# Kernel tuning notes

Hardware: AMD Instinct MI355X
Metric: run time of the kernel (lower is better)

Reference implementation:

```python
import jax, jax.numpy as jnp
import numpy as np


def setup_inputs() -> dict:
    key = jax.random.key(0)
    k1, k2, k3, k4 = jax.random.split(key, 4)
    B, H, S, D = 8, 32, 8192, 128
    query = jax.random.normal(k1, (B, H, 1, D), dtype=jnp.float32)
    key_cache = jax.random.normal(k2, (B, H, S, D), dtype=jnp.float32)
    value_cache = jax.random.normal(k3, (B, H, S, D), dtype=jnp.float32)
    W_out = jax.random.normal(k4, (H * D, H * D), dtype=jnp.float32) * (1.0 / np.sqrt(H * D))
    b_out = jnp.zeros((H * D,), dtype=jnp.float32)
    return {"query": query, "key_cache": key_cache, "value_cache": value_cache,
            "W_out": W_out, "b_out": b_out}


def reference(query, key_cache, value_cache, W_out, b_out):
    B, H, _, D = query.shape
    # scores: [B, H, 1, S]
    scores = jnp.einsum("bhqd,bhsd->bhqs", query, key_cache) / jnp.sqrt(
        jnp.asarray(D, dtype=query.dtype))
    probs = jax.nn.softmax(scores, axis=-1)
    # attn values: [B, H, 1, D]
    attn = jnp.einsum("bhqs,bhsd->bhqd", probs, value_cache)
    # [B, 1, H*D]
    attn = attn.transpose(0, 2, 1, 3).reshape(B, 1, H * D)
    # out_proj: x @ W^T + b (torch Linear convention)
    out = attn @ W_out.T + b_out
    return out
```

## Files before the change

### kernel.cpp

```cpp
#include <hip/hip_runtime.h>
#include <math.h>

#define TPB    256
#define CHUNK  1024
#define DHEAD  128
#define NB     8

__global__ __launch_bounds__(TPB) void attn_partial(
    const float* __restrict__ q, const float* __restrict__ kc,
    const float* __restrict__ vc, float* __restrict__ part,
    int S, int nsplit)
{
    const int bh    = blockIdx.x;
    const int split = blockIdx.y;
    const int tid   = threadIdx.x;
    const int s0    = split * CHUNK;

    __shared__ float sc[CHUNK];
    __shared__ float qs[DHEAD];
    __shared__ float red[8];
    __shared__ float accs[8][DHEAD];

    if (tid < DHEAD) qs[tid] = q[(size_t)bh * DHEAD + tid];
    __syncthreads();

    const int lane32 = tid & 31;
    const int grp    = tid >> 5;
    const float4 q4  = ((const float4*)qs)[lane32];
    const float scale = 0.088388347648318447f;

    const float* Kbase = kc + ((size_t)bh * S + s0) * DHEAD;
    for (int it = 0; it < CHUNK / 8; ++it) {
        const int row = it * 8 + grp;
        const float4 k4 = ((const float4*)(Kbase + (size_t)row * DHEAD))[lane32];
        float p = q4.x * k4.x + q4.y * k4.y + q4.z * k4.z + q4.w * k4.w;
        #pragma unroll
        for (int off = 16; off > 0; off >>= 1) p += __shfl_xor(p, off);
        if (lane32 == 0) sc[row] = p * scale;
    }
    __syncthreads();

    float m = -INFINITY;
    for (int i = tid; i < CHUNK; i += TPB) m = fmaxf(m, sc[i]);
    #pragma unroll
    for (int off = 32; off > 0; off >>= 1) m = fmaxf(m, __shfl_xor(m, off));
    if ((tid & 63) == 0) red[tid >> 6] = m;
    __syncthreads();
    m = fmaxf(fmaxf(red[0], red[1]), fmaxf(red[2], red[3]));

    float lsum = 0.f;
    for (int i = tid; i < CHUNK; i += TPB) {
        const float e = expf(sc[i] - m);
        sc[i] = e;
        lsum += e;
    }
    #pragma unroll
    for (int off = 32; off > 0; off >>= 1) lsum += __shfl_xor(lsum, off);
    if ((tid & 63) == 0) red[4 + (tid >> 6)] = lsum;
    __syncthreads();
    lsum = red[4] + red[5] + red[6] + red[7];

    const float* Vbase = vc + ((size_t)bh * S + s0) * DHEAD;
    float4 acc = make_float4(0.f, 0.f, 0.f, 0.f);
    const int sBeg = grp * (CHUNK / 8);
    for (int s = sBeg; s < sBeg + CHUNK / 8; ++s) {
        const float  p  = sc[s];
        const float4 v4 = ((const float4*)(Vbase + (size_t)s * DHEAD))[lane32];
        acc.x += p * v4.x; acc.y += p * v4.y;
        acc.z += p * v4.z; acc.w += p * v4.w;
    }
    ((float4*)accs[grp])[lane32] = acc;
    __syncthreads();

    float* P = part + ((size_t)bh * nsplit + split) * (DHEAD + 2);
    if (tid < DHEAD) {
        float a = 0.f;
        #pragma unroll
        for (int g = 0; g < 8; ++g) a += accs[g][tid];
        P[tid] = a;
    }
    if (tid == 0) { P[DHEAD] = m; P[DHEAD + 1] = lsum; }
}

__global__ __launch_bounds__(DHEAD) void attn_combine(
    const float* __restrict__ part, float* __restrict__ attn,
    int nsplit, int H)
{
    const int bh  = blockIdx.x;
    const int tid = threadIdx.x;
    const float* P = part + (size_t)bh * nsplit * (DHEAD + 2);

    float m = -INFINITY;
    for (int s = 0; s < nsplit; ++s)
        m = fmaxf(m, P[s * (DHEAD + 2) + DHEAD]);

    float l = 0.f, a = 0.f;
    for (int s = 0; s < nsplit; ++s) {
        const float w = expf(P[s * (DHEAD + 2) + DHEAD] - m);
        l += P[s * (DHEAD + 2) + DHEAD + 1] * w;
        a += P[s * (DHEAD + 2) + tid] * w;
    }
    attn[(size_t)bh * DHEAD + tid] = a / l;
}

__global__ __launch_bounds__(TPB) void out_proj(
    const float* __restrict__ attn, const float* __restrict__ W,
    const float* __restrict__ bias, float* __restrict__ out, int HD)
{
    const int j   = blockIdx.x;
    const int tid = threadIdx.x;
    const float4* Wr = (const float4*)(W + (size_t)j * HD);
    const int nv = HD >> 2;

    float acc[NB];
    #pragma unroll
    for (int b = 0; b < NB; ++b) acc[b] = 0.f;

    for (int i = tid; i < nv; i += TPB) {
        const float4 w4 = Wr[i];
        #pragma unroll
        for (int b = 0; b < NB; ++b) {
            const float4 a4 = ((const float4*)attn)[(size_t)b * nv + i];
            acc[b] += w4.x * a4.x + w4.y * a4.y + w4.z * a4.z + w4.w * a4.w;
        }
    }

    #pragma unroll
    for (int b = 0; b < NB; ++b) {
        #pragma unroll
        for (int off = 32; off > 0; off >>= 1)
            acc[b] += __shfl_xor(acc[b], off);
    }

    __shared__ float red[4][NB];
    if ((tid & 63) == 0) {
        #pragma unroll
        for (int b = 0; b < NB; ++b) red[tid >> 6][b] = acc[b];
    }
    __syncthreads();
    if (tid < NB) {
        const float r = red[0][tid] + red[1][tid] + red[2][tid] + red[3][tid];
        out[(size_t)tid * HD + j] = r + bias[j];
    }
}

extern "C" void kernel_launch(void* const* d_in, const int* in_sizes, int n_in,
                              void* d_out, int out_size, void* d_ws, size_t ws_size,
                              hipStream_t stream)
{
    const float* q    = (const float*)d_in[0];
    const float* kc   = (const float*)d_in[1];
    const float* vc   = (const float*)d_in[2];
    const float* W    = (const float*)d_in[3];
    const float* bias = (const float*)d_in[4];
    float* out = (float*)d_out;

    const int HD = in_sizes[4];
    const int B  = in_sizes[0] / HD;
    const int H  = HD / DHEAD;
    const int S  = in_sizes[1] / in_sizes[0];
    const int BH = B * H;
    const int nsplit = S / CHUNK;

    float* part = (float*)d_ws;
    float* attn = part + (size_t)BH * nsplit * (DHEAD + 2);

    attn_partial<<<dim3(BH, nsplit), TPB, 0, stream>>>(q, kc, vc, part, S, nsplit);
    attn_combine<<<BH, DHEAD, 0, stream>>>(part, attn, nsplit, H);
    out_proj<<<HD, TPB, 0, stream>>>(attn, W, bias, out, HD);
}
```

Baseline: 401.9 us.

## Fuse split combine into partial kernel via atomic counter; widen out_proj rows

Removes the separate combine kernel: each partial block bumps a per-head atomic counter, and the last block to finish merges all splits for that head. The K dot-product loop now handles two rows per iteration to get more loads in flight. out_proj computes four output columns per block, so each attn load is reused across four W rows. This adds a memset launch and atomics in exchange for one fewer kernel launch.

```diff
diff --git a/kernel.cpp b/kernel.cpp
--- a/kernel.cpp
+++ b/kernel.cpp
@@ -5,10 +5,13 @@
 #define CHUNK  1024
 #define DHEAD  128
 #define NB     8
+#define NJ     4
+#define PSTRIDE (DHEAD + 2)
 
 __global__ __launch_bounds__(TPB) void attn_partial(
     const float* __restrict__ q, const float* __restrict__ kc,
     const float* __restrict__ vc, float* __restrict__ part,
+    float* __restrict__ attn, unsigned int* __restrict__ cnt,
     int S, int nsplit)
 {
     const int bh    = blockIdx.x;
@@ -20,6 +23,7 @@
     __shared__ float qs[DHEAD];
     __shared__ float red[8];
     __shared__ float accs[8][DHEAD];
+    __shared__ unsigned int done_prev;
 
     if (tid < DHEAD) qs[tid] = q[(size_t)bh * DHEAD + tid];
     __syncthreads();
@@ -30,13 +34,19 @@
     const float scale = 0.088388347648318447f;
 
     const float* Kbase = kc + ((size_t)bh * S + s0) * DHEAD;
-    for (int it = 0; it < CHUNK / 8; ++it) {
-        const int row = it * 8 + grp;
-        const float4 k4 = ((const float4*)(Kbase + (size_t)row * DHEAD))[lane32];
-        float p = q4.x * k4.x + q4.y * k4.y + q4.z * k4.z + q4.w * k4.w;
-        #pragma unroll
-        for (int off = 16; off > 0; off >>= 1) p += __shfl_xor(p, off);
-        if (lane32 == 0) sc[row] = p * scale;
+    for (int it = 0; it < CHUNK / 16; ++it) {
+        const int r0 = it * 16 + grp;
+        const int r1 = r0 + 8;
+        const float4 ka = ((const float4*)(Kbase + (size_t)r0 * DHEAD))[lane32];
+        const float4 kb = ((const float4*)(Kbase + (size_t)r1 * DHEAD))[lane32];
+        float pa = q4.x * ka.x + q4.y * ka.y + q4.z * ka.z + q4.w * ka.w;
+        float pb = q4.x * kb.x + q4.y * kb.y + q4.z * kb.z + q4.w * kb.w;
+        #pragma unroll
+        for (int off = 16; off > 0; off >>= 1) {
+            pa += __shfl_xor(pa, off);
+            pb += __shfl_xor(pb, off);
+        }
+        if (lane32 == 0) { sc[r0] = pa * scale; sc[r1] = pb * scale; }
     }
     __syncthreads();
 
@@ -72,7 +82,7 @@
     ((float4*)accs[grp])[lane32] = acc;
     __syncthreads();
 
-    float* P = part + ((size_t)bh * nsplit + split) * (DHEAD + 2);
+    float* P = part + ((size_t)bh * nsplit + split) * PSTRIDE;
     if (tid < DHEAD) {
         float a = 0.f;
         #pragma unroll
@@ -80,67 +90,95 @@
         P[tid] = a;
     }
     if (tid == 0) { P[DHEAD] = m; P[DHEAD + 1] = lsum; }
-}
-
-__global__ __launch_bounds__(DHEAD) void attn_combine(
-    const float* __restrict__ part, float* __restrict__ attn,
-    int nsplit, int H)
-{
-    const int bh  = blockIdx.x;
-    const int tid = threadIdx.x;
-    const float* P = part + (size_t)bh * nsplit * (DHEAD + 2);
-
-    float m = -INFINITY;
-    for (int s = 0; s < nsplit; ++s)
-        m = fmaxf(m, P[s * (DHEAD + 2) + DHEAD]);
-
-    float l = 0.f, a = 0.f;
-    for (int s = 0; s < nsplit; ++s) {
-        const float w = expf(P[s * (DHEAD + 2) + DHEAD] - m);
-        l += P[s * (DHEAD + 2) + DHEAD + 1] * w;
-        a += P[s * (DHEAD + 2) + tid] * w;
-    }
-    attn[(size_t)bh * DHEAD + tid] = a / l;
+
+    __threadfence();
+    __syncthreads();
+    if (tid == 0) {
+        done_prev = __hip_atomic_fetch_add(&cnt[bh], 1u, __ATOMIC_ACQ_REL,
+                                           __HIP_MEMORY_SCOPE_AGENT);
+    }
+    __syncthreads();
+    if (done_prev == (unsigned)(nsplit - 1)) {
+        if (tid < DHEAD) {
+            const float* Pb = part + (size_t)bh * nsplit * PSTRIDE;
+            float gm = -INFINITY;
+            for (int s = 0; s < nsplit; ++s) {
+                const float ms = __hip_atomic_load(Pb + s * PSTRIDE + DHEAD,
+                                                   __ATOMIC_RELAXED,
+                                                   __HIP_MEMORY_SCOPE_AGENT);
+                gm = fmaxf(gm, ms);
+            }
+            float l = 0.f, a = 0.f;
+            for (int s = 0; s < nsplit; ++s) {
+                const float ms = __hip_atomic_load(Pb + s * PSTRIDE + DHEAD,
+                                                   __ATOMIC_RELAXED,
+                                                   __HIP_MEMORY_SCOPE_AGENT);
+                const float ls = __hip_atomic_load(Pb + s * PSTRIDE + DHEAD + 1,
+                                                   __ATOMIC_RELAXED,
+                                                   __HIP_MEMORY_SCOPE_AGENT);
+                const float as = __hip_atomic_load(Pb + s * PSTRIDE + tid,
+                                                   __ATOMIC_RELAXED,
+                                                   __HIP_MEMORY_SCOPE_AGENT);
+                const float w = expf(ms - gm);
+                l += ls * w;
+                a += as * w;
+            }
+            attn[(size_t)bh * DHEAD + tid] = a / l;
+        }
+    }
 }
 
 __global__ __launch_bounds__(TPB) void out_proj(
     const float* __restrict__ attn, const float* __restrict__ W,
     const float* __restrict__ bias, float* __restrict__ out, int HD)
 {
-    const int j   = blockIdx.x;
+    const int j0  = blockIdx.x * NJ;
     const int tid = threadIdx.x;
-    const float4* Wr = (const float4*)(W + (size_t)j * HD);
-    const int nv = HD >> 2;
-
-    float acc[NB];
-    #pragma unroll
-    for (int b = 0; b < NB; ++b) acc[b] = 0.f;
+    const int nv  = HD >> 2;
+    const float4* attn4 = (const float4*)attn;
+
+    float acc[NJ][NB];
+    #pragma unroll
+    for (int c = 0; c < NJ; ++c)
+        #pragma unroll
+        for (int b = 0; b < NB; ++b) acc[c][b] = 0.f;
 
     for (int i = tid; i < nv; i += TPB) {
-        const float4 w4 = Wr[i];
+        float4 w4[NJ];
+        #pragma unroll
+        for (int c = 0; c < NJ; ++c)
+            w4[c] = ((const float4*)(W + (size_t)(j0 + c) * HD))[i];
         #pragma unroll
         for (int b = 0; b < NB; ++b) {
-            const float4 a4 = ((const float4*)attn)[(size_t)b * nv + i];
-            acc[b] += w4.x * a4.x + w4.y * a4.y + w4.z * a4.z + w4.w * a4.w;
+            const float4 a4 = attn4[(size_t)b * nv + i];
+            #pragma unroll
+            for (int c = 0; c < NJ; ++c) {
+                acc[c][b] += w4[c].x * a4.x + w4[c].y * a4.y
+                           + w4[c].z * a4.z + w4[c].w * a4.w;
+            }
         }
     }
 
     #pragma unroll
-    for (int b = 0; b < NB; ++b) {
-        #pragma unroll
-        for (int off = 32; off > 0; off >>= 1)
-            acc[b] += __shfl_xor(acc[b], off);
-    }
-
-    __shared__ float red[4][NB];
+    for (int c = 0; c < NJ; ++c)
+        #pragma unroll
+        for (int b = 0; b < NB; ++b)
+            #pragma unroll
+            for (int off = 32; off > 0; off >>= 1)
+                acc[c][b] += __shfl_xor(acc[c][b], off);
+
+    __shared__ float red[4][NJ][NB];
     if ((tid & 63) == 0) {
         #pragma unroll
-        for (int b = 0; b < NB; ++b) red[tid >> 6][b] = acc[b];
-    }
-    __syncthreads();
-    if (tid < NB) {
-        const float r = red[0][tid] + red[1][tid] + red[2][tid] + red[3][tid];
-        out[(size_t)tid * HD + j] = r + bias[j];
+        for (int c = 0; c < NJ; ++c)
+            #pragma unroll
+            for (int b = 0; b < NB; ++b) red[tid >> 6][c][b] = acc[c][b];
+    }
+    __syncthreads();
+    if (tid < NJ * NB) {
+        const int c = tid >> 3, b = tid & 7;
+        const float r = red[0][c][b] + red[1][c][b] + red[2][c][b] + red[3][c][b];
+        out[(size_t)b * HD + (j0 + c)] = r + bias[j0 + c];
     }
 }
 
@@ -163,9 +201,11 @@
     const int nsplit = S / CHUNK;
 
     float* part = (float*)d_ws;
-    float* attn = part + (size_t)BH * nsplit * (DHEAD + 2);
-
-    attn_partial<<<dim3(BH, nsplit), TPB, 0, stream>>>(q, kc, vc, part, S, nsplit);
-    attn_combine<<<BH, DHEAD, 0, stream>>>(part, attn, nsplit, H);
-    out_proj<<<HD, TPB, 0, stream>>>(attn, W, bias, out, HD);
+    float* attn = part + (size_t)BH * nsplit * PSTRIDE;
+    unsigned int* cnt = (unsigned int*)(attn + (size_t)B * HD);
+
+    hipMemsetAsync(cnt, 0, (size_t)BH * sizeof(unsigned int), stream);
+    attn_partial<<<dim3(BH, nsplit), TPB, 0, stream>>>(q, kc, vc, part, attn, cnt,
+                                                       S, nsplit);
+    out_proj<<<HD / NJ, TPB, 0, stream>>>(attn, W, bias, out, HD);
 }
```

Result: slower. 852.3 us (+112.1%).
